# Kernel optimization log

Measured on AMD Instinct MI355X. Metric: run time of the kernel, lower is better.

Reference implementation:

```python
import jax, jax.numpy as jnp
import numpy as np

B = 1048576  # batch size
D = 16       # in_dim == hid_dim == out_dim (required by the torch matmul broadcasting)


def setup_inputs() -> dict:
    key = jax.random.key(0)
    kx, kw = jax.random.split(key)
    x = jax.random.normal(kx, (B, D), dtype=jnp.float32)
    W = jax.random.normal(kw, (D, D, D), dtype=jnp.float32) * (1.0 / D)
    return {"x": x, "W": W}


def reference(x, W):
    # Original torch: xBx = x @ W @ x.T permuted, then take the batch diagonal.
    # Mathematically: out[b, k] = sum_{i, j} x[b, i] * W[k, i, j] * x[b, j]
    # (batched bilinear/quadratic form per output channel k). We compute only
    # the needed diagonal terms instead of the full BxB cross-batch product.
    return jnp.einsum('bi,kij,bj->bk', x, W, x)
```

## Files before the change

kernel.cpp:

```cpp
#include <hip/hip_runtime.h>
#include <hip/hip_bf16.h>


typedef __attribute__((ext_vector_type(8)))  short  short8;
typedef __attribute__((ext_vector_type(8)))  __bf16 bf16x8;
typedef __attribute__((ext_vector_type(4)))  float  floatx4;

#define DEV static __device__ __forceinline__

constexpr int  alpha_of(int c) { return (c < 32) ? (c & 3) : (c - 32); }
constexpr int  beta_of(int c)  { return (c < 32) ? ((c & 3) + (c >> 2)) : (c - 32 + 8); }
constexpr bool live_of(int c)  { return c < 36; }

template <int C>
DEV float pval(const float* xv) {
    if constexpr (!live_of(C)) return 0.f;
    else return xv[alpha_of(C)] * xv[beta_of(C)];
}

template <int S>
DEV short8 make_afrag(const float* xv) {
    union { short8 s; __hip_bfloat162 h[4]; } u;
    u.h[0] = __float22bfloat162_rn(make_float2(pval<8 * S + 0>(xv), pval<8 * S + 1>(xv)));
    u.h[1] = __float22bfloat162_rn(make_float2(pval<8 * S + 2>(xv), pval<8 * S + 3>(xv)));
    u.h[2] = __float22bfloat162_rn(make_float2(pval<8 * S + 4>(xv), pval<8 * S + 5>(xv)));
    u.h[3] = __float22bfloat162_rn(make_float2(pval<8 * S + 6>(xv), pval<8 * S + 7>(xv)));
    return u.s;
}

DEV floatx4 mfma_bf16(short8 a, short8 b, floatx4 c) {
    return __builtin_amdgcn_mfma_f32_16x16x32_bf16(
        __builtin_bit_cast(bf16x8, a), __builtin_bit_cast(bf16x8, b), c, 0, 0, 0);
}

__global__ __launch_bounds__(256, 4)
void bilinear16_kernel(const float* __restrict__ x, const float* __restrict__ W,
                       float* __restrict__ out, int ntiles) {
    __shared__ __align__(16) short Qt[16][160];
    const int tid = threadIdx.x;
    for (int idx = tid; idx < 16 * 160; idx += 256) {
        const int n = idx / 160;
        const int k = idx - n * 160;
        const int s = k >> 5, q = (k >> 3) & 3, j = k & 7;
        const int c = 8 * s + j;
        float qv = 0.f;
        if (c < 36) {
            const int a = (c < 32) ? (c & 3) : (c - 32);
            const int b = (c < 32) ? ((c & 3) + (c >> 2)) : (c - 32 + 8);
            const float w = (c < 32) ? 1.0f : 0.5f;
            const int I = (a + 4 * q) & 15, J = (b + 4 * q) & 15;
            qv = (I == J) ? W[n * 256 + I * 16 + I]
                          : w * (W[n * 256 + I * 16 + J] + W[n * 256 + J * 16 + I]);
        }
        __hip_bfloat16 h = __float2bfloat16(qv);
        Qt[n][k] = *reinterpret_cast<short*>(&h);
    }
    __syncthreads();

    const int lane = tid & 63;
    const int n    = lane & 15;
    const int q    = lane >> 4;

    const short8 b0 = *reinterpret_cast<const short8*>(&Qt[n][0 * 32 + q * 8]);
    const short8 b1 = *reinterpret_cast<const short8*>(&Qt[n][1 * 32 + q * 8]);
    const short8 b2 = *reinterpret_cast<const short8*>(&Qt[n][2 * 32 + q * 8]);
    const short8 b3 = *reinterpret_cast<const short8*>(&Qt[n][3 * 32 + q * 8]);
    const short8 b4 = *reinterpret_cast<const short8*>(&Qt[n][4 * 32 + q * 8]);

    const int waveId = blockIdx.x * 4 + (tid >> 6);
    const int nwaves = gridDim.x * 4;

    for (int t = waveId; t < ntiles; t += nwaves) {
        const float4* xr = reinterpret_cast<const float4*>(x + (size_t)(t * 16 + n) * 16);
        const float4 c0 = xr[q];
        const float4 c1 = xr[(q + 1) & 3];
        const float4 c2 = xr[(q + 2) & 3];
        const float xv[12] = {c0.x, c0.y, c0.z, c0.w,
                              c1.x, c1.y, c1.z, c1.w,
                              c2.x, c2.y, c2.z, c2.w};

        const short8 a0 = make_afrag<0>(xv);
        const short8 a1 = make_afrag<1>(xv);
        const short8 a2 = make_afrag<2>(xv);
        const short8 a3 = make_afrag<3>(xv);
        const short8 a4 = make_afrag<4>(xv);

        floatx4 acc = {0.f, 0.f, 0.f, 0.f};
        acc = mfma_bf16(a0, b0, acc);
        acc = mfma_bf16(a1, b1, acc);
        acc = mfma_bf16(a2, b2, acc);
        acc = mfma_bf16(a3, b3, acc);
        acc = mfma_bf16(a4, b4, acc);

        float* orow = out + (size_t)(t * 16 + q * 4) * 16 + n;
        orow[0]  = acc[0];
        orow[16] = acc[1];
        orow[32] = acc[2];
        orow[48] = acc[3];
    }
}

extern "C" void kernel_launch(void* const* d_in, const int* in_sizes, int n_in,
                              void* d_out, int out_size, void* d_ws, size_t ws_size,
                              hipStream_t stream) {
    const float* x = (const float*)d_in[0];
    const float* W = (const float*)d_in[1];
    float* out = (float*)d_out;
    const int Bn = in_sizes[0] / 16;
    const int ntiles = Bn >> 4;
    bilinear16_kernel<<<2048, 256, 0, stream>>>(x, W, out, ntiles);
}
```

Before: 127.2 us.

## Precompute bf16 Q matrix in prep kernel and process four tiles per wave iteration

Adds a one-block prep kernel that builds the bf16 symmetric-packed W matrix into workspace, so each main block loads B fragments from global memory instead of rebuilding them in LDS with a barrier. The main loop now handles four 16-row tiles per iteration and issues all twelve float4 loads up front to raise memory-level parallelism. The result is an extra kernel launch and more registers per thread, and the main loop has no tail guard when ntiles is not a multiple of four. The old LDS path remains as a fallback when workspace is too small.

Measured after the change: 127.4 us. No clear change (+0.2%).

```diff
diff --git a/kernel.cpp b/kernel.cpp
--- a/kernel.cpp
+++ b/kernel.cpp
@@ -33,27 +33,93 @@
         __builtin_bit_cast(bf16x8, a), __builtin_bit_cast(bf16x8, b), c, 0, 0, 0);
 }
 
+DEV float q_elem(const float* __restrict__ W, int e) {
+    const int n = e / 160;
+    const int k = e - n * 160;
+    const int s = k >> 5, q = (k >> 3) & 3, j = k & 7;
+    const int c = 8 * s + j;
+    float qv = 0.f;
+    if (c < 36) {
+        const int a = (c < 32) ? (c & 3) : (c - 32);
+        const int b = (c < 32) ? ((c & 3) + (c >> 2)) : (c - 32 + 8);
+        const float w = (c < 32) ? 1.0f : 0.5f;
+        const int I = (a + 4 * q) & 15, J = (b + 4 * q) & 15;
+        qv = (I == J) ? W[n * 256 + I * 16 + I]
+                      : w * (W[n * 256 + I * 16 + J] + W[n * 256 + J * 16 + I]);
+    }
+    return qv;
+}
+
+__global__ void qprep_kernel(const float* __restrict__ W, short* __restrict__ Qg) {
+    for (int e = threadIdx.x; e < 16 * 160; e += 256) {
+        __hip_bfloat16 h = __float2bfloat16(q_elem(W, e));
+        Qg[e] = *reinterpret_cast<short*>(&h);
+    }
+}
+
+DEV void do_tile(const float4 c0, const float4 c1, const float4 c2,
+                 const short8 b0, const short8 b1, const short8 b2,
+                 const short8 b3, const short8 b4, float* __restrict__ ob) {
+    const float xv[12] = {c0.x, c0.y, c0.z, c0.w,
+                          c1.x, c1.y, c1.z, c1.w,
+                          c2.x, c2.y, c2.z, c2.w};
+    floatx4 acc = {0.f, 0.f, 0.f, 0.f};
+    acc = mfma_bf16(make_afrag<0>(xv), b0, acc);
+    acc = mfma_bf16(make_afrag<1>(xv), b1, acc);
+    acc = mfma_bf16(make_afrag<2>(xv), b2, acc);
+    acc = mfma_bf16(make_afrag<3>(xv), b3, acc);
+    acc = mfma_bf16(make_afrag<4>(xv), b4, acc);
+    ob[0]  = acc[0];
+    ob[16] = acc[1];
+    ob[32] = acc[2];
+    ob[48] = acc[3];
+}
+
 __global__ __launch_bounds__(256, 4)
-void bilinear16_kernel(const float* __restrict__ x, const float* __restrict__ W,
-                       float* __restrict__ out, int ntiles) {
+void bilinear16_main(const float* __restrict__ x, const short* __restrict__ Qg,
+                     float* __restrict__ out, int nbatch) {
+    const int tid  = threadIdx.x;
+    const int lane = tid & 63;
+    const int n    = lane & 15;
+    const int q    = lane >> 4;
+
+    const short8 b0 = *reinterpret_cast<const short8*>(Qg + n * 160 + 0 * 32 + q * 8);
+    const short8 b1 = *reinterpret_cast<const short8*>(Qg + n * 160 + 1 * 32 + q * 8);
+    const short8 b2 = *reinterpret_cast<const short8*>(Qg + n * 160 + 2 * 32 + q * 8);
+    const short8 b3 = *reinterpret_cast<const short8*>(Qg + n * 160 + 3 * 32 + q * 8);
+    const short8 b4 = *reinterpret_cast<const short8*>(Qg + n * 160 + 4 * 32 + q * 8);
+
+    const int waveId = blockIdx.x * 4 + (tid >> 6);
+    const int nwaves = gridDim.x * 4;
+
+    for (int g = waveId; g < nbatch; g += nwaves) {
+        const size_t t0 = (size_t)g * 4;
+        const float4* xA = reinterpret_cast<const float4*>(x + t0 * 256) + n * 4;
+        const float4* A0 = xA + ((q + 0) & 3);
+        const float4* A1 = xA + ((q + 1) & 3);
+        const float4* A2 = xA + ((q + 2) & 3);
+
+        const float4 c00 = A0[0],   c01 = A1[0],   c02 = A2[0];
+        const float4 c10 = A0[64],  c11 = A1[64],  c12 = A2[64];
+        const float4 c20 = A0[128], c21 = A1[128], c22 = A2[128];
+        const float4 c30 = A0[192], c31 = A1[192], c32 = A2[192];
+
+        float* ob = out + t0 * 256 + q * 64 + n;
+        do_tile(c00, c01, c02, b0, b1, b2, b3, b4, ob);
+        do_tile(c10, c11, c12, b0, b1, b2, b3, b4, ob + 256);
+        do_tile(c20, c21, c22, b0, b1, b2, b3, b4, ob + 512);
+        do_tile(c30, c31, c32, b0, b1, b2, b3, b4, ob + 768);
+    }
+}
+
+__global__ __launch_bounds__(256, 4)
+void bilinear16_lds(const float* __restrict__ x, const float* __restrict__ W,
+                    float* __restrict__ out, int ntiles) {
     __shared__ __align__(16) short Qt[16][160];
     const int tid = threadIdx.x;
-    for (int idx = tid; idx < 16 * 160; idx += 256) {
-        const int n = idx / 160;
-        const int k = idx - n * 160;
-        const int s = k >> 5, q = (k >> 3) & 3, j = k & 7;
-        const int c = 8 * s + j;
-        float qv = 0.f;
-        if (c < 36) {
-            const int a = (c < 32) ? (c & 3) : (c - 32);
-            const int b = (c < 32) ? ((c & 3) + (c >> 2)) : (c - 32 + 8);
-            const float w = (c < 32) ? 1.0f : 0.5f;
-            const int I = (a + 4 * q) & 15, J = (b + 4 * q) & 15;
-            qv = (I == J) ? W[n * 256 + I * 16 + I]
-                          : w * (W[n * 256 + I * 16 + J] + W[n * 256 + J * 16 + I]);
-        }
-        __hip_bfloat16 h = __float2bfloat16(qv);
-        Qt[n][k] = *reinterpret_cast<short*>(&h);
+    for (int e = tid; e < 16 * 160; e += 256) {
+        __hip_bfloat16 h = __float2bfloat16(q_elem(W, e));
+        Qt[0][e] = *reinterpret_cast<short*>(&h);
     }
     __syncthreads();
 
@@ -75,28 +141,8 @@
         const float4 c0 = xr[q];
         const float4 c1 = xr[(q + 1) & 3];
         const float4 c2 = xr[(q + 2) & 3];
-        const float xv[12] = {c0.x, c0.y, c0.z, c0.w,
-                              c1.x, c1.y, c1.z, c1.w,
-                              c2.x, c2.y, c2.z, c2.w};
-
-        const short8 a0 = make_afrag<0>(xv);
-        const short8 a1 = make_afrag<1>(xv);
-        const short8 a2 = make_afrag<2>(xv);
-        const short8 a3 = make_afrag<3>(xv);
-        const short8 a4 = make_afrag<4>(xv);
-
-        floatx4 acc = {0.f, 0.f, 0.f, 0.f};
-        acc = mfma_bf16(a0, b0, acc);
-        acc = mfma_bf16(a1, b1, acc);
-        acc = mfma_bf16(a2, b2, acc);
-        acc = mfma_bf16(a3, b3, acc);
-        acc = mfma_bf16(a4, b4, acc);
-
-        float* orow = out + (size_t)(t * 16 + q * 4) * 16 + n;
-        orow[0]  = acc[0];
-        orow[16] = acc[1];
-        orow[32] = acc[2];
-        orow[48] = acc[3];
+        float* ob = out + (size_t)t * 256 + q * 64 + n;
+        do_tile(c0, c1, c2, b0, b1, b2, b3, b4, ob);
     }
 }
 
@@ -108,5 +154,13 @@
     float* out = (float*)d_out;
     const int Bn = in_sizes[0] / 16;
     const int ntiles = Bn >> 4;
-    bilinear16_kernel<<<2048, 256, 0, stream>>>(x, W, out, ntiles);
+
+    if (ws_size >= (size_t)(16 * 160 * sizeof(short))) {
+        short* Qg = (short*)d_ws;
+        qprep_kernel<<<1, 256, 0, stream>>>(W, Qg);
+        const int nbatch = (ntiles + 3) >> 2;
+        bilinear16_main<<<2048, 256, 0, stream>>>(x, Qg, out, nbatch);
+    } else {
+        bilinear16_lds<<<2048, 256, 0, stream>>>(x, W, out, ntiles);
+    }
 }
```
